# Kernel tuning notes

Measured on AMD Instinct MI355X. Metric: run time of the kernel, lower is better.

The kernel has to match this reference:

```python
import jax, jax.numpy as jnp
import numpy as np

B, D, L, N, M, K = 256, 512, 196, 1024, 512, 10000  # batch, context, num_ctx, hidden, embed, vocab


def setup_inputs() -> dict:
    key = jax.random.key(0)
    ks = jax.random.split(key, 20)
    r = lambda k, s: jax.random.normal(k, s, dtype=jnp.float32) * 0.02
    return {
        "a_i": jax.random.normal(ks[0], (B, D, L), dtype=jnp.float32),
        "inp": jax.random.normal(ks[1], (B, 1, K), dtype=jnp.float32),
        "hn_prev": jax.random.normal(ks[2], (B, 1, N), dtype=jnp.float32),
        "cn_prev": jax.random.normal(ks[3], (B, 1, N), dtype=jnp.float32),
        "f_att_w": r(ks[4], (N + D,)),  # Linear(n+D -> 1), stored as a vector
        "f_att_b": r(ks[5], (1,)),
        "gate_w": r(ks[6], (N,)),       # Linear(n -> 1)
        "gate_b": r(ks[7], (1,)),
        "E_w": r(ks[8], (M, K)),        # torch Linear weight [out, in]
        "E_b": r(ks[9], (M,)),
        "W_ih": r(ks[10], (4 * N, D + N + M)),  # LSTM input->hidden (i,f,g,o)
        "W_hh": r(ks[11], (4 * N, N)),
        "b_ih": r(ks[12], (4 * N,)),
        "b_hh": r(ks[13], (4 * N,)),
        "Lh_w": r(ks[14], (M, N)),
        "Lh_b": r(ks[15], (M,)),
        "Lz_w": r(ks[16], (M, D)),
        "Lz_b": r(ks[17], (M,)),
        "Lo_w": r(ks[18], (K, M)),
        "Lo_b": r(ks[19], (K,)),
    }


def reference(a_i, inp, hn_prev, cn_prev,
              f_att_w, f_att_b, gate_w, gate_b,
              E_w, E_b, W_ih, W_hh, b_ih, b_hh,
              Lh_w, Lh_b, Lz_w, Lz_b, Lo_w, Lo_b):
    h = hn_prev[:, 0]  # [B, N]
    c = cn_prev[:, 0]  # [B, N]
    # --- additive attention: the 196-iteration torch loop batched into one einsum ---
    # cat((a_i[:,:,i], h)) @ f_att_w splits into the a-part and h-part of the weight.
    w_a, w_h = f_att_w[:D], f_att_w[D:]
    e = jnp.einsum('bdl,d->bl', a_i, w_a) + (h @ w_h)[:, None] + f_att_b  # [B, L]
    alpha = jax.nn.softmax(e, axis=1)                                     # [B, L]
    beta = jax.nn.sigmoid(h @ gate_w + gate_b)                            # [B]
    z = beta[:, None] * jnp.einsum('bl,bdl->bd', alpha, a_i)              # [B, D]
    # --- word embedding ---
    w_emb = inp[:, 0] @ E_w.T + E_b                                       # [B, M]
    # --- single-step LSTM (PyTorch gate order i, f, g, o) ---
    x = jnp.concatenate([w_emb, h, z], axis=1)                            # [B, M+N+D]
    gates = x @ W_ih.T + b_ih + h @ W_hh.T + b_hh                         # [B, 4N]
    i_g, f_g, g_g, o_g = jnp.split(gates, 4, axis=1)
    cn = jax.nn.sigmoid(f_g) * c + jax.nn.sigmoid(i_g) * jnp.tanh(g_g)
    hn = jax.nn.sigmoid(o_g) * jnp.tanh(cn)
    # --- output projection ---
    deep_out = w_emb + (hn @ Lh_w.T + Lh_b) + (z @ Lz_w.T + Lz_b)         # [B, M]
    p_yt = deep_out @ Lo_w.T + Lo_b                                       # [B, K]
    return (p_yt[:, None, :], hn[:, None, :], cn[:, None, :], alpha[:, None, :])
```

## Files before the change

kernel.cpp:

```cpp
#include <hip/hip_runtime.h>
#include <hip/hip_bf16.h>
#include <math.h>

#define BB 256
#define DD 512
#define LL 196
#define NN 1024
#define MM 512
#define KK 10000

#define OUT_PY 0
#define OUT_HN ((size_t)2560000)
#define OUT_CN ((size_t)2822144)
#define OUT_AL ((size_t)3084288)

#define OFF_PE     ((size_t)0)
#define OFF_BETA   ((size_t)802816)
#define OFF_EMB    ((size_t)803072)
#define OFF_EMBP   ((size_t)934144)
#define OFF_GATESP ((size_t)3031296)
#define OFF_DP     ((size_t)11419904)
#define OFF_EWB    ((size_t)14565632)
#define OFF_WIHB   ((size_t)17125632)
#define OFF_WHHB   ((size_t)21319936)
#define OFF_LHB    ((size_t)23417088)
#define OFF_LZB    ((size_t)23679232)
#define OFF_LOB    ((size_t)23810304)
#define OFF_INPB   ((size_t)26370304)
#define OFF_HB     ((size_t)27650304)
#define OFF_ZB     ((size_t)27781376)
#define OFF_EMBB   ((size_t)27846912)
#define OFF_DEEPB  ((size_t)27912448)
#define OFF_HNB    ((size_t)27977984)

typedef __attribute__((ext_vector_type(8))) short short8v;
typedef __attribute__((ext_vector_type(4))) float f32x4;

__device__ __forceinline__ unsigned short f2bf(float f) {
    unsigned int u = __builtin_bit_cast(unsigned int, f);
    u += 0x7fffu + ((u >> 16) & 1u);
    return (unsigned short)(u >> 16);
}

__device__ __forceinline__ void gl_lds16(const float* g, float* l) {
    __builtin_amdgcn_global_load_lds(
        (const __attribute__((address_space(1))) void*)g,
        (__attribute__((address_space(3))) void*)l, 16, 0, 0);
}

__device__ __forceinline__ short8v stage8b(const unsigned short* __restrict__ p,
                                           bool ok, int kbase, int Ktot) {
    if (ok && (kbase + 7 < Ktot)) return *(const short8v*)(p + kbase);
    short8v v;
#pragma unroll
    for (int i = 0; i < 8; ++i) {
        const int k = kbase + i;
        v[i] = (ok && k < Ktot) ? (short)p[k] : (short)0;
    }
    return v;
}

struct GSrc { const unsigned short* A; int lda; const unsigned short* B; int ldb; int ktn; int K; };

__device__ __forceinline__ void gemm_body(
    const int bx, const int by, const int bz, const int rowBlocks,
    const GSrc s1, const GSrc s2,
    float* __restrict__ C, const int ldc, const int Ncols,
    const int ktPerSplit, const float* __restrict__ bias,
    short (*As)[64][72], short (*Bs)[64][72])
{
    const int t = threadIdx.x;
    const int row0 = bx * 64;
    const int col0 = by * 64;
    const int ktTot = s1.ktn + s2.ktn;
    const int kt0 = bz * ktPerSplit;
    const int nk = min(ktTot, kt0 + ktPerSplit) - kt0;

    const int sr = t >> 2;
    const int sk = (t & 3) << 4;
    const int bc = col0 + sr;
    const bool bok = (bc < Ncols);
    const unsigned short* aP1 = s1.A + (size_t)(row0 + sr) * s1.lda;
    const unsigned short* bP1 = s1.B + (size_t)(bok ? bc : 0) * s1.ldb;
    const unsigned short* aP2 = s2.A ? (s2.A + (size_t)(row0 + sr) * s2.lda) : aP1;
    const unsigned short* bP2 = s2.A ? (s2.B + (size_t)(bok ? bc : 0) * s2.ldb) : bP1;

    const int l = t & 63, w = t >> 6;
    const int wrow = (w >> 1) * 32, wcol = (w & 1) * 32;
    const int lr = l & 15, g = l >> 4, g8 = g * 8;

    f32x4 acc[2][2] = {};

    short8v sa0, sa1, sb0, sb1;
    {
        const int ktg = kt0;
        const unsigned short* aR; const unsigned short* bR; int kk, Kt;
        if (ktg < s1.ktn) { aR = aP1; bR = bP1; kk = (ktg << 6) + sk; Kt = s1.K; }
        else              { aR = aP2; bR = bP2; kk = ((ktg - s1.ktn) << 6) + sk; Kt = s2.K; }
        sa0 = stage8b(aR, true, kk, Kt);  sa1 = stage8b(aR, true, kk + 8, Kt);
        sb0 = stage8b(bR, bok,  kk, Kt);  sb1 = stage8b(bR, bok,  kk + 8, Kt);
    }
    *(short8v*)&As[0][sr][sk] = sa0; *(short8v*)&As[0][sr][sk + 8] = sa1;
    *(short8v*)&Bs[0][sr][sk] = sb0; *(short8v*)&Bs[0][sr][sk + 8] = sb1;
    __syncthreads();

    int cur = 0;
    for (int kt = 0; kt < nk; ++kt) {
        const bool more = (kt + 1 < nk);
        if (more) {
            const int ktg = kt0 + kt + 1;
            const unsigned short* aR; const unsigned short* bR; int kk, Kt;
            if (ktg < s1.ktn) { aR = aP1; bR = bP1; kk = (ktg << 6) + sk; Kt = s1.K; }
            else              { aR = aP2; bR = bP2; kk = ((ktg - s1.ktn) << 6) + sk; Kt = s2.K; }
            sa0 = stage8b(aR, true, kk, Kt);  sa1 = stage8b(aR, true, kk + 8, Kt);
            sb0 = stage8b(bR, bok,  kk, Kt);  sb1 = stage8b(bR, bok,  kk + 8, Kt);
        }
#pragma unroll
        for (int ks = 0; ks < 2; ++ks) {
            const int ko = ks * 32 + g8;
            short8v a0 = *(const short8v*)&As[cur][wrow + lr][ko];
            short8v a1 = *(const short8v*)&As[cur][wrow + 16 + lr][ko];
            short8v b0 = *(const short8v*)&Bs[cur][wcol + lr][ko];
            short8v b1 = *(const short8v*)&Bs[cur][wcol + 16 + lr][ko];
            acc[0][0] = __builtin_amdgcn_mfma_f32_16x16x32_bf16(a0, b0, acc[0][0], 0, 0, 0);
            acc[0][1] = __builtin_amdgcn_mfma_f32_16x16x32_bf16(a0, b1, acc[0][1], 0, 0, 0);
            acc[1][0] = __builtin_amdgcn_mfma_f32_16x16x32_bf16(a1, b0, acc[1][0], 0, 0, 0);
            acc[1][1] = __builtin_amdgcn_mfma_f32_16x16x32_bf16(a1, b1, acc[1][1], 0, 0, 0);
        }
        if (more) {
            *(short8v*)&As[cur ^ 1][sr][sk] = sa0;
            *(short8v*)&As[cur ^ 1][sr][sk + 8] = sa1;
            *(short8v*)&Bs[cur ^ 1][sr][sk] = sb0;
            *(short8v*)&Bs[cur ^ 1][sr][sk + 8] = sb1;
        }
        __syncthreads();
        cur ^= 1;
    }

    float* Cp = C + (size_t)bz * ((size_t)rowBlocks * 64) * ldc;
#pragma unroll
    for (int m = 0; m < 2; ++m)
#pragma unroll
        for (int n = 0; n < 2; ++n)
#pragma unroll
            for (int j = 0; j < 4; ++j) {
                const int r = row0 + wrow + m * 16 + g * 4 + j;
                const int c = col0 + wcol + n * 16 + lr;
                if (c < Ncols) {
                    float v = acc[m][n][j];
                    if (bias) v += bias[c];
                    Cp[(size_t)r * ldc + c] = v;
                }
            }
}

#define CVT_NBLK 1615
__global__ __launch_bounds__(256) void l1_atte_cvt(
    const float* __restrict__ a_i, const float* __restrict__ f_att_w,
    float* __restrict__ pe,
    const float* __restrict__ E_w, const float* __restrict__ W_ih,
    const float* __restrict__ W_hh, const float* __restrict__ Lh_w,
    const float* __restrict__ Lz_w, const float* __restrict__ Lo_w,
    const float* __restrict__ inp, const float* __restrict__ h,
    unsigned short* __restrict__ ewb, unsigned short* __restrict__ wihb,
    unsigned short* __restrict__ whhb, unsigned short* __restrict__ lhb,
    unsigned short* __restrict__ lzb, unsigned short* __restrict__ lob,
    unsigned short* __restrict__ inpb, unsigned short* __restrict__ hb)
{
    __shared__ __align__(16) float slab[6280];
    const int bid = blockIdx.x;
    const int t = threadIdx.x;

    if (bid < 4096) {
        const int b = bid >> 4, ch = bid & 15;
        const int w = t >> 6, lane = t & 63;
        const float* gbase = a_i + ((size_t)b * DD + ch * 32) * LL;
#pragma unroll
        for (int k = 0; k < 7; ++k) {
            const int cw = k * 256 + w * 64;
            if (cw + lane < 1568)
                gl_lds16(gbase + (size_t)(cw + lane) * 4, slab + (size_t)cw * 4);
        }
        if (t < 8) slab[6272 + t] = 0.f;
        asm volatile("s_waitcnt vmcnt(0)" ::: "memory");
        __syncthreads();
        if (t < LL) {
            const float* wp = f_att_w + ch * 32;
            float e = 0.f;
#pragma unroll
            for (int d = 0; d < 32; ++d) e += slab[d * LL + t] * wp[d];
            pe[((size_t)b * 16 + ch) * LL + t] = e;
        }
    } else {
        int lb = bid - 4096;
        const float* src; unsigned short* dst; int n;
        if      (lb < 313)  {             src = E_w;  dst = ewb;  n = 5120000; }
        else if (lb < 825)  { lb -= 313;  src = W_ih; dst = wihb; n = 8388608; }
        else if (lb < 1081) { lb -= 825;  src = W_hh; dst = whhb; n = 4194304; }
        else if (lb < 1113) { lb -= 1081; src = Lh_w; dst = lhb;  n = 524288; }
        else if (lb < 1129) { lb -= 1113; src = Lz_w; dst = lzb;  n = 262144; }
        else if (lb < 1442) { lb -= 1129; src = Lo_w; dst = lob;  n = 5120000; }
        else if (lb < 1599) { lb -= 1442; src = inp;  dst = inpb; n = 2560000; }
        else                { lb -= 1599; src = h;    dst = hb;   n = 262144; }
#pragma unroll
        for (int i = 0; i < 8; ++i) {
            const size_t e = (size_t)lb * 16384 + (size_t)i * 2048 + (size_t)t * 8;
            if (e + 8 <= (size_t)n) {
                const float4 x = *(const float4*)(src + e);
                const float4 y = *(const float4*)(src + e + 4);
                short8v v;
                v[0] = (short)f2bf(x.x); v[1] = (short)f2bf(x.y);
                v[2] = (short)f2bf(x.z); v[3] = (short)f2bf(x.w);
                v[4] = (short)f2bf(y.x); v[5] = (short)f2bf(y.y);
                v[6] = (short)f2bf(y.z); v[7] = (short)f2bf(y.w);
                *(short8v*)(dst + e) = v;
            }
        }
    }
}

__global__ __launch_bounds__(256) void l2_emb_gatesh(
    const unsigned short* __restrict__ inpb, const unsigned short* __restrict__ ewb,
    float* __restrict__ embp,
    const unsigned short* __restrict__ hb, const unsigned short* __restrict__ wihb,
    const unsigned short* __restrict__ whhb, float* __restrict__ gatesp)
{
    __shared__ __align__(16) short As[2][64][72];
    __shared__ __align__(16) short Bs[2][64][72];
    const int bid = blockIdx.x;
    if (bid < 512) {
        GSrc s1 = {inpb, KK, ewb, KK, 157, KK};
        GSrc s2 = {nullptr, 0, nullptr, 0, 0, 0};
        gemm_body(bid & 3, (bid >> 2) & 7, bid >> 5, 4, s1, s2,
                  embp, MM, MM, 10, nullptr, As, Bs);
    } else {
        const int i = bid - 512;
        GSrc s1 = {hb, NN, wihb + 512, 2048, 16, NN};
        GSrc s2 = {hb, NN, whhb, NN, 16, NN};
        gemm_body(i & 3, (i >> 2) & 63, i >> 8, 4, s1, s2,
                  gatesp, 4096, 4096, 8, nullptr, As, Bs);
    }
}

__global__ __launch_bounds__(256) void l3_softmax_embred(
    const float* __restrict__ pe, const float* __restrict__ h,
    const float* __restrict__ f_att_w, const float* __restrict__ f_att_b,
    const float* __restrict__ gate_w, const float* __restrict__ gate_b,
    float* __restrict__ alpha_out, float* __restrict__ beta,
    const float* __restrict__ embp, const float* __restrict__ E_b,
    float* __restrict__ emb, unsigned short* __restrict__ embb)
{
    const int bid = blockIdx.x;
    const int t = threadIdx.x;
    if (bid < 256) {
        const int b = bid;
        __shared__ float red[256];
        __shared__ float red2[256];
        const float4 h4 = *(const float4*)(h + (size_t)b * NN + t * 4);
        const float4 w4 = *(const float4*)(f_att_w + DD + t * 4);
        const float4 g4 = *(const float4*)(gate_w + t * 4);
        float hd = h4.x * w4.x + h4.y * w4.y + h4.z * w4.z + h4.w * w4.w;
        float gd = h4.x * g4.x + h4.y * g4.y + h4.z * g4.z + h4.w * g4.w;
        red[t] = hd; red2[t] = gd;
        __syncthreads();
        for (int s = 128; s > 0; s >>= 1) {
            if (t < s) { red[t] += red[t + s]; red2[t] += red2[t + s]; }
            __syncthreads();
        }
        const float hdot = red[0];
        const float gdot = red2[0];
        __syncthreads();
        float e = -3.4e38f;
        if (t < LL) {
            const float* p = pe + (size_t)b * 16 * LL + t;
            e = hdot + f_att_b[0];
#pragma unroll
            for (int ch = 0; ch < 16; ++ch) e += p[ch * LL];
        }
        red[t] = e;
        __syncthreads();
        for (int s = 128; s > 0; s >>= 1) {
            if (t < s) red[t] = fmaxf(red[t], red[t + s]);
            __syncthreads();
        }
        const float mx = red[0];
        __syncthreads();
        const float ex = (t < LL) ? expf(e - mx) : 0.f;
        red[t] = ex;
        __syncthreads();
        for (int s = 128; s > 0; s >>= 1) {
            if (t < s) red[t] += red[t + s];
            __syncthreads();
        }
        const float inv = 1.f / red[0];
        if (t < LL) alpha_out[(size_t)b * LL + t] = ex * inv;
        if (t == 0) beta[b] = 1.f / (1.f + expf(-(gdot + gate_b[0])));
    } else {
        const int idx = (bid - 256) * 256 + t;
        const int j = idx & 511;
        float v = E_b[j];
#pragma unroll
        for (int s = 0; s < 16; ++s) v += embp[(size_t)s * (BB * 512) + idx];
        emb[idx] = v;
        embb[idx] = f2bf(v);
    }
}

__global__ __launch_bounds__(256) void l4_attz(
    const float* __restrict__ a_i, const float* __restrict__ alpha,
    const float* __restrict__ beta, unsigned short* __restrict__ zb)
{
    __shared__ __align__(16) float slab[6280];
    __shared__ float al[200];
    const int t = threadIdx.x;
    const int b = blockIdx.x >> 4, ch = blockIdx.x & 15;
    const int w = t >> 6, lane = t & 63;
    const float* gbase = a_i + ((size_t)b * DD + ch * 32) * LL;
#pragma unroll
    for (int k = 0; k < 7; ++k) {
        const int cw = k * 256 + w * 64;
        if (cw + lane < 1568)
            gl_lds16(gbase + (size_t)(cw + lane) * 4, slab + (size_t)cw * 4);
    }
    if (t < 200) al[t] = (t < LL) ? alpha[(size_t)b * LL + t] : 0.f;
    if (t < 8) slab[6272 + t] = 0.f;
    asm volatile("s_waitcnt vmcnt(0)" ::: "memory");
    __syncthreads();
    const int r = t >> 3, q = t & 7;
    const float* rowp = slab + r * LL + q * 25;
    const float* alq  = al + q * 25;
    float s = 0.f;
#pragma unroll
    for (int j = 0; j < 25; ++j) s += rowp[j] * alq[j];
    s += __shfl_xor(s, 1, 64);
    s += __shfl_xor(s, 2, 64);
    s += __shfl_xor(s, 4, 64);
    if (q == 0) zb[(size_t)b * DD + ch * 32 + r] = f2bf(beta[b] * s);
}

__global__ __launch_bounds__(256) void l5_gatesez_lz(
    const unsigned short* __restrict__ embb, const unsigned short* __restrict__ zb,
    const unsigned short* __restrict__ wihb, float* __restrict__ gatesp,
    const unsigned short* __restrict__ lzb, float* __restrict__ dp)
{
    __shared__ __align__(16) short As[2][64][72];
    __shared__ __align__(16) short Bs[2][64][72];
    const int bid = blockIdx.x;
    if (bid < 512) {
        GSrc s1 = {embb, MM, wihb, 2048, 8, MM};
        GSrc s2 = {nullptr, 0, nullptr, 0, 0, 0};
        gemm_body(bid & 3, (bid >> 2) & 63, bid >> 8, 4, s1, s2,
                  gatesp + (size_t)4 * BB * 4096, 4096, 4096, 4, nullptr, As, Bs);
    } else if (bid < 1024) {
        const int i = bid - 512;
        GSrc s1 = {zb, DD, wihb + 1536, 2048, 8, DD};
        GSrc s2 = {nullptr, 0, nullptr, 0, 0, 0};
        gemm_body(i & 3, (i >> 2) & 63, i >> 8, 4, s1, s2,
                  gatesp + (size_t)6 * BB * 4096, 4096, 4096, 4, nullptr, As, Bs);
    } else {
        const int i = bid - 1024;
        GSrc s1 = {zb, DD, lzb, DD, 8, DD};
        GSrc s2 = {nullptr, 0, nullptr, 0, 0, 0};
        gemm_body(i & 3, (i >> 2) & 7, i >> 5, 4, s1, s2,
                  dp, MM, MM, 1, nullptr, As, Bs);
    }
}

__global__ __launch_bounds__(256) void l6_lstm(
    const float* __restrict__ gatesp,
    const float* __restrict__ b_ih, const float* __restrict__ b_hh,
    const float* __restrict__ c_prev, float* __restrict__ hn, float* __restrict__ cn,
    unsigned short* __restrict__ hnb)
{
    const int idx = blockIdx.x * 256 + threadIdx.x;
    const int b = idx >> 10, n = idx & 1023;
    float g[4];
#pragma unroll
    for (int gi = 0; gi < 4; ++gi) {
        const int col = gi * 1024 + n;
        const size_t o = (size_t)b * 4096 + col;
        float v = b_ih[col] + b_hh[col];
#pragma unroll
        for (int s = 0; s < 8; ++s) v += gatesp[(size_t)s * (BB * 4096) + o];
        g[gi] = v;
    }
    const float si = 1.f / (1.f + expf(-g[0]));
    const float sf = 1.f / (1.f + expf(-g[1]));
    const float so = 1.f / (1.f + expf(-g[3]));
    const float tg = tanhf(g[2]);
    const float c = c_prev[idx];
    const float cnv = sf * c + si * tg;
    const float hnv = so * tanhf(cnv);
    cn[idx] = cnv;
    hn[idx] = hnv;
    hnb[idx] = f2bf(hnv);
}

__global__ __launch_bounds__(256) void l7_lh(
    const unsigned short* __restrict__ hnb, const unsigned short* __restrict__ lhb,
    float* __restrict__ dp_hi)
{
    __shared__ __align__(16) short As[2][64][72];
    __shared__ __align__(16) short Bs[2][64][72];
    const int bid = blockIdx.x;
    GSrc s1 = {hnb, NN, lhb, NN, 16, NN};
    GSrc s2 = {nullptr, 0, nullptr, 0, 0, 0};
    gemm_body(bid & 3, (bid >> 2) & 7, bid >> 5, 4, s1, s2,
              dp_hi, MM, MM, 1, nullptr, As, Bs);
}

__global__ __launch_bounds__(256) void l8_deep(
    const float* __restrict__ emb, const float* __restrict__ dp,
    const float* __restrict__ Lh_b, const float* __restrict__ Lz_b,
    unsigned short* __restrict__ deepb)
{
    const int idx = blockIdx.x * 256 + threadIdx.x;
    const int j = idx & 511;
    float v = emb[idx] + Lh_b[j] + Lz_b[j];
#pragma unroll
    for (int s = 0; s < 24; ++s) v += dp[(size_t)s * (BB * 512) + idx];
    deepb[idx] = f2bf(v);
}

__global__ __launch_bounds__(256) void l9_pyt(
    const unsigned short* __restrict__ deepb, const unsigned short* __restrict__ lob,
    const float* __restrict__ Lo_b, float* __restrict__ out)
{
    __shared__ __align__(16) short As[2][64][72];
    __shared__ __align__(16) short Bs[2][64][72];
    const int bid = blockIdx.x;
    GSrc s1 = {deepb, MM, lob, MM, 8, MM};
    GSrc s2 = {nullptr, 0, nullptr, 0, 0, 0};
    gemm_body(bid & 3, bid >> 2, 0, 4, s1, s2,
              out, KK, KK, 8, Lo_b, As, Bs);
}

extern "C" void kernel_launch(void* const* d_in, const int* in_sizes, int n_in,
                              void* d_out, int out_size, void* d_ws, size_t ws_size,
                              hipStream_t stream)
{
    const float* a_i     = (const float*)d_in[0];
    const float* inp     = (const float*)d_in[1];
    const float* hn_prev = (const float*)d_in[2];
    const float* cn_prev = (const float*)d_in[3];
    const float* f_att_w = (const float*)d_in[4];
    const float* f_att_b = (const float*)d_in[5];
    const float* gate_w  = (const float*)d_in[6];
    const float* gate_b  = (const float*)d_in[7];
    const float* E_w     = (const float*)d_in[8];
    const float* E_b     = (const float*)d_in[9];
    const float* W_ih    = (const float*)d_in[10];
    const float* W_hh    = (const float*)d_in[11];
    const float* b_ih    = (const float*)d_in[12];
    const float* b_hh    = (const float*)d_in[13];
    const float* Lh_w    = (const float*)d_in[14];
    const float* Lh_b    = (const float*)d_in[15];
    const float* Lz_w    = (const float*)d_in[16];
    const float* Lz_b    = (const float*)d_in[17];
    const float* Lo_w    = (const float*)d_in[18];
    const float* Lo_b    = (const float*)d_in[19];

    float* out = (float*)d_out;
    float* ws  = (float*)d_ws;

    float* PE     = ws + OFF_PE;
    float* BETA   = ws + OFF_BETA;
    float* EMB    = ws + OFF_EMB;
    float* EMBP   = ws + OFF_EMBP;
    float* GATESP = ws + OFF_GATESP;
    float* DP     = ws + OFF_DP;
    unsigned short* EWB   = (unsigned short*)(ws + OFF_EWB);
    unsigned short* WIHB  = (unsigned short*)(ws + OFF_WIHB);
    unsigned short* WHHB  = (unsigned short*)(ws + OFF_WHHB);
    unsigned short* LHB   = (unsigned short*)(ws + OFF_LHB);
    unsigned short* LZB   = (unsigned short*)(ws + OFF_LZB);
    unsigned short* LOB   = (unsigned short*)(ws + OFF_LOB);
    unsigned short* INPB  = (unsigned short*)(ws + OFF_INPB);
    unsigned short* HB    = (unsigned short*)(ws + OFF_HB);
    unsigned short* ZB    = (unsigned short*)(ws + OFF_ZB);
    unsigned short* EMBB  = (unsigned short*)(ws + OFF_EMBB);
    unsigned short* DEEPB = (unsigned short*)(ws + OFF_DEEPB);
    unsigned short* HNB   = (unsigned short*)(ws + OFF_HNB);

    l1_atte_cvt<<<4096 + CVT_NBLK, 256, 0, stream>>>(
        a_i, f_att_w, PE,
        E_w, W_ih, W_hh, Lh_w, Lz_w, Lo_w, inp, hn_prev,
        EWB, WIHB, WHHB, LHB, LZB, LOB, INPB, HB);

    l2_emb_gatesh<<<1536, 256, 0, stream>>>(INPB, EWB, EMBP,
                                            HB, WIHB, WHHB, GATESP);

    l3_softmax_embred<<<768, 256, 0, stream>>>(PE, hn_prev, f_att_w, f_att_b,
                                               gate_w, gate_b, out + OUT_AL, BETA,
                                               EMBP, E_b, EMB, EMBB);

    l4_attz<<<4096, 256, 0, stream>>>(a_i, out + OUT_AL, BETA, ZB);

    l5_gatesez_lz<<<1280, 256, 0, stream>>>(EMBB, ZB, WIHB, GATESP, LZB, DP);

    l6_lstm<<<1024, 256, 0, stream>>>(GATESP, b_ih, b_hh, cn_prev,
                                      out + OUT_HN, out + OUT_CN, HNB);

    l7_lh<<<512, 256, 0, stream>>>(HNB, LHB, DP + (size_t)8 * BB * 512);

    l8_deep<<<512, 256, 0, stream>>>(EMB, DP, Lh_b, Lz_b, DEEPB);

    l9_pyt<<<628, 256, 0, stream>>>(DEEPB, LOB, Lo_b, out + OUT_PY);
}
```

Baseline: 138.5 us.

## Spread weight conversions across kernels and merge launches to cut kernel count

Splits the bf16 weight conversion into three groups and places each group in the kernel just before the one that uses it, so conversion blocks share the grid with the attention, embedding and softmax work. The W_hh/h gates GEMM moves into the same launch as the other gate and Lz GEMMs, and attention-z, embedding reduction and the late-weight conversions share one launch. Launches drop from nine to eight, and the aim is to fill idle CUs and shorten the dependency chain. Kernels with mixed roles now use a shared LDS buffer sized for the largest role, which may lower occupancy for the lighter blocks.

```diff
diff --git a/kernel.cpp b/kernel.cpp
--- a/kernel.cpp
+++ b/kernel.cpp
@@ -48,6 +48,25 @@
         (__attribute__((address_space(3))) void*)l, 16, 0, 0);
 }
 
+__device__ __forceinline__ void cvt_body(int lb, const float* __restrict__ src,
+                                         unsigned short* __restrict__ dst, int n,
+                                         int t) {
+#pragma unroll
+    for (int i = 0; i < 8; ++i) {
+        const size_t e = (size_t)lb * 16384 + (size_t)i * 2048 + (size_t)t * 8;
+        if (e + 8 <= (size_t)n) {
+            const float4 x = *(const float4*)(src + e);
+            const float4 y = *(const float4*)(src + e + 4);
+            short8v v;
+            v[0] = (short)f2bf(x.x); v[1] = (short)f2bf(x.y);
+            v[2] = (short)f2bf(x.z); v[3] = (short)f2bf(x.w);
+            v[4] = (short)f2bf(y.x); v[5] = (short)f2bf(y.y);
+            v[6] = (short)f2bf(y.z); v[7] = (short)f2bf(y.w);
+            *(short8v*)(dst + e) = v;
+        }
+    }
+}
+
 __device__ __forceinline__ short8v stage8b(const unsigned short* __restrict__ p,
                                            bool ok, int kbase, int Ktot) {
     if (ok && (kbase + 7 < Ktot)) return *(const short8v*)(p + kbase);
@@ -154,18 +173,13 @@
             }
 }
 
-#define CVT_NBLK 1615
-__global__ __launch_bounds__(256) void l1_atte_cvt(
+__global__ __launch_bounds__(256) void m1_atte_cvt1(
     const float* __restrict__ a_i, const float* __restrict__ f_att_w,
     float* __restrict__ pe,
-    const float* __restrict__ E_w, const float* __restrict__ W_ih,
-    const float* __restrict__ W_hh, const float* __restrict__ Lh_w,
-    const float* __restrict__ Lz_w, const float* __restrict__ Lo_w,
-    const float* __restrict__ inp, const float* __restrict__ h,
-    unsigned short* __restrict__ ewb, unsigned short* __restrict__ wihb,
-    unsigned short* __restrict__ whhb, unsigned short* __restrict__ lhb,
-    unsigned short* __restrict__ lzb, unsigned short* __restrict__ lob,
-    unsigned short* __restrict__ inpb, unsigned short* __restrict__ hb)
+    const float* __restrict__ E_w, const float* __restrict__ inp,
+    const float* __restrict__ h,
+    unsigned short* __restrict__ ewb, unsigned short* __restrict__ inpb,
+    unsigned short* __restrict__ hb)
 {
     __shared__ __align__(16) float slab[6280];
     const int bid = blockIdx.x;
@@ -193,69 +207,29 @@
         }
     } else {
         int lb = bid - 4096;
-        const float* src; unsigned short* dst; int n;
-        if      (lb < 313)  {             src = E_w;  dst = ewb;  n = 5120000; }
-        else if (lb < 825)  { lb -= 313;  src = W_ih; dst = wihb; n = 8388608; }
-        else if (lb < 1081) { lb -= 825;  src = W_hh; dst = whhb; n = 4194304; }
-        else if (lb < 1113) { lb -= 1081; src = Lh_w; dst = lhb;  n = 524288; }
-        else if (lb < 1129) { lb -= 1113; src = Lz_w; dst = lzb;  n = 262144; }
-        else if (lb < 1442) { lb -= 1129; src = Lo_w; dst = lob;  n = 5120000; }
-        else if (lb < 1599) { lb -= 1442; src = inp;  dst = inpb; n = 2560000; }
-        else                { lb -= 1599; src = h;    dst = hb;   n = 262144; }
-#pragma unroll
-        for (int i = 0; i < 8; ++i) {
-            const size_t e = (size_t)lb * 16384 + (size_t)i * 2048 + (size_t)t * 8;
-            if (e + 8 <= (size_t)n) {
-                const float4 x = *(const float4*)(src + e);
-                const float4 y = *(const float4*)(src + e + 4);
-                short8v v;
-                v[0] = (short)f2bf(x.x); v[1] = (short)f2bf(x.y);
-                v[2] = (short)f2bf(x.z); v[3] = (short)f2bf(x.w);
-                v[4] = (short)f2bf(y.x); v[5] = (short)f2bf(y.y);
-                v[6] = (short)f2bf(y.z); v[7] = (short)f2bf(y.w);
-                *(short8v*)(dst + e) = v;
-            }
-        }
-    }
-}
-
-__global__ __launch_bounds__(256) void l2_emb_gatesh(
-    const unsigned short* __restrict__ inpb, const unsigned short* __restrict__ ewb,
-    float* __restrict__ embp,
-    const unsigned short* __restrict__ hb, const unsigned short* __restrict__ wihb,
-    const unsigned short* __restrict__ whhb, float* __restrict__ gatesp)
-{
-    __shared__ __align__(16) short As[2][64][72];
-    __shared__ __align__(16) short Bs[2][64][72];
-    const int bid = blockIdx.x;
-    if (bid < 512) {
-        GSrc s1 = {inpb, KK, ewb, KK, 157, KK};
-        GSrc s2 = {nullptr, 0, nullptr, 0, 0, 0};
-        gemm_body(bid & 3, (bid >> 2) & 7, bid >> 5, 4, s1, s2,
-                  embp, MM, MM, 10, nullptr, As, Bs);
-    } else {
-        const int i = bid - 512;
-        GSrc s1 = {hb, NN, wihb + 512, 2048, 16, NN};
-        GSrc s2 = {hb, NN, whhb, NN, 16, NN};
-        gemm_body(i & 3, (i >> 2) & 63, i >> 8, 4, s1, s2,
-                  gatesp, 4096, 4096, 8, nullptr, As, Bs);
-    }
-}
-
-__global__ __launch_bounds__(256) void l3_softmax_embred(
+        if      (lb < 313) cvt_body(lb, E_w, ewb, 5120000, t);
+        else if (lb < 470) cvt_body(lb - 313, inp, inpb, 2560000, t);
+        else               cvt_body(lb - 470, h, hb, 262144, t);
+    }
+}
+
+__global__ __launch_bounds__(256) void m2_softmax_emb_cvt2(
     const float* __restrict__ pe, const float* __restrict__ h,
     const float* __restrict__ f_att_w, const float* __restrict__ f_att_b,
     const float* __restrict__ gate_w, const float* __restrict__ gate_b,
     float* __restrict__ alpha_out, float* __restrict__ beta,
-    const float* __restrict__ embp, const float* __restrict__ E_b,
-    float* __restrict__ emb, unsigned short* __restrict__ embb)
-{
+    const unsigned short* __restrict__ inpb, const unsigned short* __restrict__ ewb,
+    float* __restrict__ embp,
+    const float* __restrict__ W_ih, const float* __restrict__ W_hh,
+    unsigned short* __restrict__ wihb, unsigned short* __restrict__ whhb)
+{
+    __shared__ __align__(16) unsigned char smem[36864];
     const int bid = blockIdx.x;
     const int t = threadIdx.x;
     if (bid < 256) {
         const int b = bid;
-        __shared__ float red[256];
-        __shared__ float red2[256];
+        float* red  = (float*)smem;
+        float* red2 = red + 256;
         const float4 h4 = *(const float4*)(h + (size_t)b * NN + t * 4);
         const float4 w4 = *(const float4*)(f_att_w + DD + t * 4);
         const float4 g4 = *(const float4*)(gate_w + t * 4);
@@ -295,70 +269,106 @@
         const float inv = 1.f / red[0];
         if (t < LL) alpha_out[(size_t)b * LL + t] = ex * inv;
         if (t == 0) beta[b] = 1.f / (1.f + expf(-(gdot + gate_b[0])));
+    } else if (bid < 768) {
+        short (*As)[64][72] = (short (*)[64][72])smem;
+        short (*Bs)[64][72] = (short (*)[64][72])(smem + 18432);
+        const int i = bid - 256;
+        GSrc s1 = {inpb, KK, ewb, KK, 157, KK};
+        GSrc s2 = {nullptr, 0, nullptr, 0, 0, 0};
+        gemm_body(i & 3, (i >> 2) & 7, i >> 5, 4, s1, s2,
+                  embp, MM, MM, 10, nullptr, As, Bs);
     } else {
-        const int idx = (bid - 256) * 256 + t;
+        int lb = bid - 768;
+        if (lb < 512) cvt_body(lb, W_ih, wihb, 8388608, t);
+        else          cvt_body(lb - 512, W_hh, whhb, 4194304, t);
+    }
+}
+
+__global__ __launch_bounds__(256) void m3_attz_embred_cvt3(
+    const float* __restrict__ a_i, const float* __restrict__ alpha,
+    const float* __restrict__ beta, unsigned short* __restrict__ zb,
+    const float* __restrict__ embp, const float* __restrict__ E_b,
+    float* __restrict__ emb, unsigned short* __restrict__ embb,
+    const float* __restrict__ Lo_w, const float* __restrict__ Lh_w,
+    const float* __restrict__ Lz_w,
+    unsigned short* __restrict__ lob, unsigned short* __restrict__ lhb,
+    unsigned short* __restrict__ lzb)
+{
+    __shared__ __align__(16) float slab[6280];
+    __shared__ float al[200];
+    const int bid = blockIdx.x;
+    const int t = threadIdx.x;
+
+    if (bid < 4096) {
+        const int b = bid >> 4, ch = bid & 15;
+        const int w = t >> 6, lane = t & 63;
+        const float* gbase = a_i + ((size_t)b * DD + ch * 32) * LL;
+#pragma unroll
+        for (int k = 0; k < 7; ++k) {
+            const int cw = k * 256 + w * 64;
+            if (cw + lane < 1568)
+                gl_lds16(gbase + (size_t)(cw + lane) * 4, slab + (size_t)cw * 4);
+        }
+        if (t < 200) al[t] = (t < LL) ? alpha[(size_t)b * LL + t] : 0.f;
+        if (t < 8) slab[6272 + t] = 0.f;
+        asm volatile("s_waitcnt vmcnt(0)" ::: "memory");
+        __syncthreads();
+        const int r = t >> 3, q = t & 7;
+        const float* rowp = slab + r * LL + q * 25;
+        const float* alq  = al + q * 25;
+        float s = 0.f;
+#pragma unroll
+        for (int j = 0; j < 25; ++j) s += rowp[j] * alq[j];
+        s += __shfl_xor(s, 1, 64);
+        s += __shfl_xor(s, 2, 64);
+        s += __shfl_xor(s, 4, 64);
+        if (q == 0) zb[(size_t)b * DD + ch * 32 + r] = f2bf(beta[b] * s);
+    } else if (bid < 4608) {
+        const int idx = (bid - 4096) * 256 + t;
         const int j = idx & 511;
         float v = E_b[j];
 #pragma unroll
         for (int s = 0; s < 16; ++s) v += embp[(size_t)s * (BB * 512) + idx];
         emb[idx] = v;
         embb[idx] = f2bf(v);
-    }
-}
-
-__global__ __launch_bounds__(256) void l4_attz(
-    const float* __restrict__ a_i, const float* __restrict__ alpha,
-    const float* __restrict__ beta, unsigned short* __restrict__ zb)
-{
-    __shared__ __align__(16) float slab[6280];
-    __shared__ float al[200];
-    const int t = threadIdx.x;
-    const int b = blockIdx.x >> 4, ch = blockIdx.x & 15;
-    const int w = t >> 6, lane = t & 63;
-    const float* gbase = a_i + ((size_t)b * DD + ch * 32) * LL;
-#pragma unroll
-    for (int k = 0; k < 7; ++k) {
-        const int cw = k * 256 + w * 64;
-        if (cw + lane < 1568)
-            gl_lds16(gbase + (size_t)(cw + lane) * 4, slab + (size_t)cw * 4);
-    }
-    if (t < 200) al[t] = (t < LL) ? alpha[(size_t)b * LL + t] : 0.f;
-    if (t < 8) slab[6272 + t] = 0.f;
-    asm volatile("s_waitcnt vmcnt(0)" ::: "memory");
-    __syncthreads();
-    const int r = t >> 3, q = t & 7;
-    const float* rowp = slab + r * LL + q * 25;
-    const float* alq  = al + q * 25;
-    float s = 0.f;
-#pragma unroll
-    for (int j = 0; j < 25; ++j) s += rowp[j] * alq[j];
-    s += __shfl_xor(s, 1, 64);
-    s += __shfl_xor(s, 2, 64);
-    s += __shfl_xor(s, 4, 64);
-    if (q == 0) zb[(size_t)b * DD + ch * 32 + r] = f2bf(beta[b] * s);
-}
-
-__global__ __launch_bounds__(256) void l5_gatesez_lz(
-    const unsigned short* __restrict__ embb, const unsigned short* __restrict__ zb,
-    const unsigned short* __restrict__ wihb, float* __restrict__ gatesp,
+    } else {
+        int lb = bid - 4608;
+        if      (lb < 313) cvt_body(lb, Lo_w, lob, 5120000, t);
+        else if (lb < 345) cvt_body(lb - 313, Lh_w, lhb, 524288, t);
+        else               cvt_body(lb - 345, Lz_w, lzb, 262144, t);
+    }
+}
+
+__global__ __launch_bounds__(256) void m4_gates_lz(
+    const unsigned short* __restrict__ hb, const unsigned short* __restrict__ embb,
+    const unsigned short* __restrict__ zb,
+    const unsigned short* __restrict__ wihb, const unsigned short* __restrict__ whhb,
+    float* __restrict__ gatesp,
     const unsigned short* __restrict__ lzb, float* __restrict__ dp)
 {
-    __shared__ __align__(16) short As[2][64][72];
-    __shared__ __align__(16) short Bs[2][64][72];
+    __shared__ __align__(16) unsigned char smem[36864];
+    short (*As)[64][72] = (short (*)[64][72])smem;
+    short (*Bs)[64][72] = (short (*)[64][72])(smem + 18432);
     const int bid = blockIdx.x;
-    if (bid < 512) {
+    if (bid < 1024) {
+        GSrc s1 = {hb, NN, wihb + 512, 2048, 16, NN};
+        GSrc s2 = {hb, NN, whhb, NN, 16, NN};
+        gemm_body(bid & 3, (bid >> 2) & 63, bid >> 8, 4, s1, s2,
+                  gatesp, 4096, 4096, 8, nullptr, As, Bs);
+    } else if (bid < 1536) {
+        const int i = bid - 1024;
         GSrc s1 = {embb, MM, wihb, 2048, 8, MM};
         GSrc s2 = {nullptr, 0, nullptr, 0, 0, 0};
-        gemm_body(bid & 3, (bid >> 2) & 63, bid >> 8, 4, s1, s2,
+        gemm_body(i & 3, (i >> 2) & 63, i >> 8, 4, s1, s2,
                   gatesp + (size_t)4 * BB * 4096, 4096, 4096, 4, nullptr, As, Bs);
-    } else if (bid < 1024) {
-        const int i = bid - 512;
+    } else if (bid < 2048) {
+        const int i = bid - 1536;
         GSrc s1 = {zb, DD, wihb + 1536, 2048, 8, DD};
         GSrc s2 = {nullptr, 0, nullptr, 0, 0, 0};
         gemm_body(i & 3, (i >> 2) & 63, i >> 8, 4, s1, s2,
                   gatesp + (size_t)6 * BB * 4096, 4096, 4096, 4, nullptr, As, Bs);
     } else {
-        const int i = bid - 1024;
+        const int i = bid - 2048;
         GSrc s1 = {zb, DD, lzb, DD, 8, DD};
         GSrc s2 = {nullptr, 0, nullptr, 0, 0, 0};
         gemm_body(i & 3, (i >> 2) & 7, i >> 5, 4, s1, s2,
@@ -366,7 +376,7 @@
     }
 }
 
-__global__ __launch_bounds__(256) void l6_lstm(
+__global__ __launch_bounds__(256) void m5_lstm(
     const float* __restrict__ gatesp,
     const float* __restrict__ b_ih, const float* __restrict__ b_hh,
     const float* __restrict__ c_prev, float* __restrict__ hn, float* __restrict__ cn,
@@ -396,7 +406,7 @@
     hnb[idx] = f2bf(hnv);
 }
 
-__global__ __launch_bounds__(256) void l7_lh(
+__global__ __launch_bounds__(256) void m6_lh(
     const unsigned short* __restrict__ hnb, const unsigned short* __restrict__ lhb,
     float* __restrict__ dp_hi)
 {
@@ -409,7 +419,7 @@
               dp_hi, MM, MM, 1, nullptr, As, Bs);
 }
 
-__global__ __launch_bounds__(256) void l8_deep(
+__global__ __launch_bounds__(256) void m7_deep(
     const float* __restrict__ emb, const float* __restrict__ dp,
     const float* __restrict__ Lh_b, const float* __restrict__ Lz_b,
     unsigned short* __restrict__ deepb)
@@ -422,7 +432,7 @@
     deepb[idx] = f2bf(v);
 }
 
-__global__ __launch_bounds__(256) void l9_pyt(
+__global__ __launch_bounds__(256) void m8_pyt(
     const unsigned short* __restrict__ deepb, const unsigned short* __restrict__ lob,
     const float* __restrict__ Lo_b, float* __restrict__ out)
 {
@@ -482,28 +492,26 @@
     unsigned short* DEEPB = (unsigned short*)(ws + OFF_DEEPB);
     unsigned short* HNB   = (unsigned short*)(ws + OFF_HNB);
 
-    l1_atte_cvt<<<4096 + CVT_NBLK, 256, 0, stream>>>(
-        a_i, f_att_w, PE,
-        E_w, W_ih, W_hh, Lh_w, Lz_w, Lo_w, inp, hn_prev,
-        EWB, WIHB, WHHB, LHB, LZB, LOB, INPB, HB);
-
-    l2_emb_gatesh<<<1536, 256, 0, stream>>>(INPB, EWB, EMBP,
-                                            HB, WIHB, WHHB, GATESP);
-
-    l3_softmax_embred<<<768, 256, 0, stream>>>(PE, hn_prev, f_att_w, f_att_b,
-                                               gate_w, gate_b, out + OUT_AL, BETA,
-                                               EMBP, E_b, EMB, EMBB);
-
-    l4_attz<<<4096, 256, 0, stream>>>(a_i, out + OUT_AL, BETA, ZB);
-
-    l5_gatesez_lz<<<1280, 256, 0, stream>>>(EMBB, ZB, WIHB, GATESP, LZB, DP);
-
-    l6_lstm<<<1024, 256, 0, stream>>>(GATESP, b_ih, b_hh, cn_prev,
+    m1_atte_cvt1<<<4582, 256, 0, stream>>>(a_i, f_att_w, PE,
+                                           E_w, inp, hn_prev, EWB, INPB, HB);
+
+    m2_softmax_emb_cvt2<<<1536, 256, 0, stream>>>(
+        PE, hn_prev, f_att_w, f_att_b, gate_w, gate_b,
+        out + OUT_AL, BETA, INPB, EWB, EMBP, W_ih, W_hh, WIHB, WHHB);
+
+    m3_attz_embred_cvt3<<<4969, 256, 0, stream>>>(
+        a_i, out + OUT_AL, BETA, ZB, EMBP, E_b, EMB, EMBB,
+        Lo_w, Lh_w, Lz_w, LOB, LHB, LZB);
+
+    m4_gates_lz<<<2304, 256, 0, stream>>>(HB, EMBB, ZB, WIHB, WHHB,
+                                          GATESP, LZB, DP);
+
+    m5_lstm<<<1024, 256, 0, stream>>>(GATESP, b_ih, b_hh, cn_prev,
                                       out + OUT_HN, out + OUT_CN, HNB);
 
-    l7_lh<<<512, 256, 0, stream>>>(HNB, LHB, DP + (size_t)8 * BB * 512);
-
-    l8_deep<<<512, 256, 0, stream>>>(EMB, DP, Lh_b, Lz_b, DEEPB);
-
-    l9_pyt<<<628, 256, 0, stream>>>(DEEPB, LOB, Lo_b, out + OUT_PY);
-}
+    m6_lh<<<512, 256, 0, stream>>>(HNB, LHB, DP + (size_t)8 * BB * 512);
+
+    m7_deep<<<512, 256, 0, stream>>>(EMB, DP, Lh_b, Lz_b, DEEPB);
+
+    m8_pyt<<<628, 256, 0, stream>>>(DEEPB, LOB, Lo_b, out + OUT_PY);
+}
```

New measurement: 137.0 us. No clear change (-1.1%).
